# Kernel tuning notes

Measured on AMD Instinct MI355X. Metric: run time of the kernel, lower is better.

The kernel has to match this reference:

```python
import jax, jax.numpy as jnp
import numpy as np

B, N, C = 32, 4097, 256  # N odd so threshold length (N+1)//2 == N//2+1 rfft bins
F = N // 2 + 1


def setup_inputs() -> dict:
    key = jax.random.key(0)
    k1, k2, k3, k4 = jax.random.split(key, 4)
    x_in = jax.random.normal(k1, (B, N, C), dtype=jnp.float32)
    # trunc_normal(std=0.02) ~ scaled normal for reference purposes
    complex_weight = jax.random.normal(k2, (C, 2), dtype=jnp.float32) * 0.02
    complex_weight_high = jax.random.normal(k3, (C, 2), dtype=jnp.float32) * 0.02
    threshold_param = jax.random.uniform(k4, (F,), dtype=jnp.float32)
    return {
        "x_in": x_in,
        "complex_weight": complex_weight,
        "complex_weight_high": complex_weight_high,
        "threshold_param": threshold_param,
    }


def reference(x_in, complex_weight, complex_weight_high, threshold_param):
    dtype = x_in.dtype
    x = x_in.astype(jnp.float32)
    x_fft = jnp.fft.rfft(x, axis=1, norm="ortho")  # [B, F, C] complex64

    weight = complex_weight[:, 0] + 1j * complex_weight[:, 1]  # [C]
    x_weighted = x_fft * weight

    # adaptive high-frequency mask (straight-through on threshold_param)
    energy = jnp.sum(jnp.abs(x_fft) ** 2, axis=-1)  # [B, F]
    median_energy = jnp.median(energy, axis=1, keepdims=True)  # [B, 1] (F odd -> exact middle, matches torch)
    normalized_energy = energy / (median_energy + 1e-6)
    hard = (normalized_energy > threshold_param).astype(jnp.float32)  # [B, F]
    adaptive_mask = jax.lax.stop_gradient(hard - threshold_param) + threshold_param

    weight_high = complex_weight_high[:, 0] + 1j * complex_weight_high[:, 1]  # [C]
    x_weighted = x_weighted + x_fft * adaptive_mask[..., None] * weight_high

    out = jnp.fft.irfft(x_weighted, n=N, axis=1, norm="ortho")  # [B, N, C]
    return out.astype(dtype)
```

## Files before the change

### kernel.cpp

```cpp
#include <hip/hip_runtime.h>
#include <math.h>
#include <float.h>

#define B_ 32
#define N_ 4097
#define C_ 256
#define F_ 2049
#define N2_ 241
#define Q_ 512
#define TWROWS 4352
#define INV_SQRT_N 0.0156230927f
#define W_N 0.0015336063f
#define W_17 0.36959913571644626f

typedef __attribute__((ext_vector_type(8))) short short8v;
typedef _Float16 f16x8 __attribute__((ext_vector_type(8)));
typedef __attribute__((ext_vector_type(4))) float f32x4;

__device__ __forceinline__ float bf2f(unsigned short u) {
    return __uint_as_float(((unsigned)u) << 16);
}
__device__ __forceinline__ unsigned short f2bf(float v) {
    unsigned u = __float_as_uint(v);
    u += 0x7FFFu + ((u >> 16) & 1u);
    return (unsigned short)(u >> 16);
}
__device__ __forceinline__ unsigned short f2h(float v) {
    union { _Float16 h; unsigned short u; } cv;
    cv.h = (_Float16)v;
    return cv.u;
}
__device__ __forceinline__ void gload16(const void* gptr, void* ldsptr) {
    __builtin_amdgcn_global_load_lds(
        (const __attribute__((address_space(1))) void*)gptr,
        (__attribute__((address_space(3))) void*)ldsptr,
        16, 0, 0);
}

__global__ __launch_bounds__(256) void k_stageA_t(const float* __restrict__ x,
                                                  unsigned short* __restrict__ yt) {
    int bid = blockIdx.x;
    int b = bid >> 5; int rem = bid & 31;
    int n2t = rem >> 2, ct = rem & 3;
    int tid = threadIdx.x;
    int cl = tid & 63, sub = tid >> 6;
    int c = ct * 64 + cl;

    float C17[17], S17[17];
#pragma unroll
    for (int r = 0; r < 17; ++r) {
        float s, cth; sincosf(W_17 * (float)r, &s, &cth);
        C17[r] = cth; S17[r] = s;
    }

    float ar[9][8], ai[8][8];
#pragma unroll
    for (int k = 0; k < 9; ++k)
#pragma unroll
        for (int i = 0; i < 8; ++i) ar[k][i] = 0.f;
#pragma unroll
    for (int k = 0; k < 8; ++k)
#pragma unroll
        for (int i = 0; i < 8; ++i) ai[k][i] = 0.f;

    const float* xb = x + (size_t)b * N_ * C_ + c;
#pragma unroll
    for (int n1 = 0; n1 < 17; ++n1) {
        float xv[8];
#pragma unroll
        for (int i = 0; i < 8; ++i) {
            int n2 = n2t * 32 + sub * 8 + i;
            xv[i] = (n2 <= 240) ? xb[(size_t)(n1 * N2_ + n2) * C_] : 0.f;
        }
#pragma unroll
        for (int k1 = 0; k1 < 9; ++k1) {
            int r = (k1 * n1) % 17;
            float cc = C17[r], ss = S17[r];
#pragma unroll
            for (int i = 0; i < 8; ++i) {
                ar[k1][i] += xv[i] * cc;
                if (k1 > 0) ai[k1 - 1][i] += xv[i] * ss;
            }
        }
    }

    __shared__ float lre[32 * 65], lim[32 * 65];
    int c2 = tid >> 2, qg = tid & 3;
#pragma unroll
    for (int j = 0; j < 9; ++j) {
        __syncthreads();
#pragma unroll
        for (int i = 0; i < 8; ++i) {
            int row = sub * 8 + i;
            lre[row * 65 + cl] = ar[j][i] * INV_SQRT_N;
            lim[row * 65 + cl] = (j > 0) ? (-ai[j - 1][i] * INV_SQRT_N) : 0.f;
        }
        __syncthreads();
        unsigned wh[8];
#pragma unroll
        for (int i = 0; i < 8; ++i) {
            int row = qg * 8 + i;
            float re = lre[row * 65 + c2], im = lim[row * 65 + c2];
            wh[i] = (unsigned)f2h(re) | ((unsigned)f2h(im) << 16);
        }
        size_t ubase = ((size_t)((b * 9 + j) * 256 + ct * 64 + c2)) * 256 + n2t * 32 + qg * 8;
        uint4 v0; v0.x = wh[0]; v0.y = wh[1]; v0.z = wh[2]; v0.w = wh[3];
        uint4 v1; v1.x = wh[4]; v1.y = wh[5]; v1.z = wh[6]; v1.w = wh[7];
        *(uint4*)((unsigned*)yt + ubase) = v0;
        *(uint4*)((unsigned*)yt + ubase + 4) = v1;
    }
}

__global__ __launch_bounds__(256) void k_twfill_all(unsigned short* __restrict__ twA,
                                                    unsigned short* __restrict__ twB) {
    int blk = blockIdx.x;
    if (blk < TWROWS) {
        int n = blk;
        int k2 = threadIdx.x;
        unsigned pack = 0u;
        if (n <= 4096 && k2 <= 240) {
            int rr = (n * k2) % N_;
            float s, cth; sincosf(W_N * (float)rr, &s, &cth);
            pack = (unsigned)f2bf(cth) | ((unsigned)f2bf(-s) << 16);
        }
        *(unsigned*)(twA + (size_t)n * Q_ + 2 * k2) = pack;
    } else {
        int idx = blk - TWROWS;
        int m = idx & 255; int k1 = idx >> 8;
        int n2 = threadIdx.x;
        int t = m >> 1, r = m & 1;
        int f = k1 + 17 * t;
        unsigned ph = 0u;
        if (t <= 120 && f < F_ && n2 <= 240) {
            float s_ = (k1 <= 8) ? 1.f : -1.f;
            int rr = (f * n2) % N_;
            float sn, cs; sincosf(W_N * (float)rr, &sn, &cs);
            float a0 = (r == 0) ? cs : -sn;
            float a1 = (r == 0) ? s_ * sn : s_ * cs;
            ph = (unsigned)f2h(a0) | ((unsigned)f2h(a1) << 16);
        }
        size_t ub = ((size_t)(k1 * 256 + m)) * 256 + n2;
        *((unsigned*)twB + ub) = ph;
    }
}

__global__ __launch_bounds__(256) void k_stageB_v4(
        const unsigned short* __restrict__ yt, const unsigned short* __restrict__ twb,
        unsigned short* __restrict__ X, float* __restrict__ energy) {
    int bid = (blockIdx.x & 7) * 272 + (blockIdx.x >> 3);
    int b = bid / 68, rem = bid % 68;
    int j, mt, ct;
    if (rem < 4) { j = 0; mt = rem >> 1; ct = rem & 1; }
    else { int r2 = rem - 4; j = 1 + (r2 >> 3); int sub = r2 & 7; mt = sub >> 1; ct = sub & 1; }
    int k1 = (mt < 2) ? j : 17 - j;
    int mh = mt & 1;
    const unsigned short* pA = twb + (size_t)(k1 * 256 + mh * 128) * Q_;
    const unsigned short* pB = yt + (size_t)((b * 9 + j) * 256 + ct * 128) * Q_;

    int tid = threadIdx.x, lane = tid & 63, wid = tid >> 6;
    int wr = wid >> 1, wc = wid & 1;
    int l15 = lane & 15, lg = lane >> 4;
    int srow = lane >> 3, sch = lane & 7;

    __shared__ __align__(16) unsigned short lds[16384];
    __shared__ float eL[2][2][4][4][2];

    f32x4 acc[4][4];
#pragma unroll
    for (int rt = 0; rt < 4; ++rt)
#pragma unroll
        for (int nt = 0; nt < 4; ++nt) acc[rt][nt] = (f32x4){0.f, 0.f, 0.f, 0.f};

    for (int ks = 0; ks < 8; ++ks) {
        int q0 = ks * 64;
#pragma unroll
        for (int r = 0; r < 8; ++r) {
            int row = (r & 3) * 32 + wid * 8 + srow;
            int ch = sch ^ ((row >> 1) & 7);
            const unsigned short* g = (r < 4) ? (pA + (size_t)row * Q_ + q0 + ch * 8)
                                              : (pB + (size_t)row * Q_ + q0 + ch * 8);
            gload16(g, &lds[(r * 4 + wid) * 512]);
        }
        __syncthreads();
        f16x8 a[2][4], bb[2][4];
#pragma unroll
        for (int rt = 0; rt < 4; ++rt) {
            int row = wr * 64 + rt * 16 + l15;
            int s = (row >> 1) & 7;
            a[0][rt] = *(const f16x8*)&lds[(row * 8 + (lg ^ s)) * 8];
            a[1][rt] = *(const f16x8*)&lds[(row * 8 + ((4 + lg) ^ s)) * 8];
        }
#pragma unroll
        for (int nt = 0; nt < 4; ++nt) {
            int row = wc * 64 + nt * 16 + l15;
            int s = (row >> 1) & 7;
            bb[0][nt] = *(const f16x8*)&lds[8192 + (row * 8 + (lg ^ s)) * 8];
            bb[1][nt] = *(const f16x8*)&lds[8192 + (row * 8 + ((4 + lg) ^ s)) * 8];
        }
#pragma unroll
        for (int kh = 0; kh < 2; ++kh)
#pragma unroll
            for (int rt = 0; rt < 4; ++rt)
#pragma unroll
                for (int nt = 0; nt < 4; ++nt)
                    acc[rt][nt] = __builtin_amdgcn_mfma_f32_16x16x32_f16(
                        a[kh][rt], bb[kh][nt], acc[rt][nt], 0, 0, 0);
        __syncthreads();
    }

#pragma unroll
    for (int rt = 0; rt < 4; ++rt) {
        float e0 = 0.f, e1 = 0.f;
#pragma unroll
        for (int nt = 0; nt < 4; ++nt) {
            e0 += acc[rt][nt][0] * acc[rt][nt][0] + acc[rt][nt][1] * acc[rt][nt][1];
            e1 += acc[rt][nt][2] * acc[rt][nt][2] + acc[rt][nt][3] * acc[rt][nt][3];
        }
#pragma unroll
        for (int off = 1; off < 16; off <<= 1) {
            e0 += __shfl_xor(e0, off, 64);
            e1 += __shfl_xor(e1, off, 64);
        }
        if (l15 == 0) { eL[wr][wc][rt][lg][0] = e0; eL[wr][wc][rt][lg][1] = e1; }
    }
    __syncthreads();
    if (tid < 64) {
        int wr2 = tid >> 5, rt2 = (tid >> 3) & 3, lg2 = (tid >> 1) & 3, pr = tid & 1;
        int mrow = mh * 128 + wr2 * 64 + rt2 * 16 + lg2 * 4 + pr * 2;
        int f = k1 + 17 * (mrow >> 1);
        if (f < F_) {
            float e = eL[wr2][0][rt2][lg2][pr] + eL[wr2][1][rt2][lg2][pr];
            atomicAdd(&energy[b * F_ + f], e);
        }
    }

#pragma unroll
    for (int rt = 0; rt < 4; ++rt) {
#pragma unroll
        for (int jj = 0; jj < 4; ++jj) {
            int mrow = mh * 128 + wr * 64 + rt * 16 + lg * 4 + jj;
            int t = mrow >> 1, p = mrow & 1;
            int f = k1 + 17 * t;
            if (f < F_) {
                size_t base = ((size_t)((b * F_ + f) * 2 + p)) * C_ + ct * 128 + wc * 64 + l15;
#pragma unroll
                for (int nt = 0; nt < 4; ++nt)
                    X[base + nt * 16] = f2bf(acc[rt][nt][jj]);
            }
        }
    }
}

__global__ __launch_bounds__(256) void k_median(const float* __restrict__ energy,
                                                float* __restrict__ med) {
    int b = blockIdx.x, tid = threadIdx.x;
    __shared__ unsigned vals[F_];
    __shared__ unsigned hist[256];
    __shared__ unsigned scanbuf[256];
    __shared__ unsigned sh_prefix;
    __shared__ int sh_rank;
    for (int i = tid; i < F_; i += 256)
        vals[i] = __float_as_uint(energy[b * F_ + i]);
    if (tid == 0) { sh_prefix = 0u; sh_rank = 1024; }
    __syncthreads();
#pragma unroll
    for (int shift = 24; shift >= 0; shift -= 8) {
        hist[tid] = 0u;
        __syncthreads();
        unsigned prefix = sh_prefix;
        unsigned hmask = (shift == 24) ? 0u : (0xFFFFFFFFu << (shift + 8));
        for (int i = tid; i < F_; i += 256) {
            unsigned v = vals[i];
            if (((v ^ prefix) & hmask) == 0u)
                atomicAdd(&hist[(v >> shift) & 255], 1u);
        }
        __syncthreads();
        scanbuf[tid] = hist[tid];
        __syncthreads();
#pragma unroll
        for (int off = 1; off < 256; off <<= 1) {
            unsigned y = (tid >= off) ? scanbuf[tid - off] : 0u;
            __syncthreads();
            scanbuf[tid] += y;
            __syncthreads();
        }
        int rank = sh_rank;
        unsigned cumP = (tid == 0) ? 0u : scanbuf[tid - 1];
        unsigned cumI = scanbuf[tid];
        __syncthreads();
        if ((unsigned)rank >= cumP && (unsigned)rank < cumI) {
            sh_prefix = prefix | ((unsigned)tid << shift);
            sh_rank = rank - (int)cumP;
        }
        __syncthreads();
    }
    if (tid == 0) med[b] = __uint_as_float(sh_prefix);
}

__global__ __launch_bounds__(256) void k_vbuild_t(
        const unsigned short* __restrict__ X, const float* __restrict__ energy,
        const float* __restrict__ med, const float* __restrict__ thr,
        const float* __restrict__ cw, const float* __restrict__ cwh,
        unsigned short* __restrict__ vt) {
    int bid = blockIdx.x;
    int b = bid >> 7; int rem = bid & 127;
    int kt = rem >> 3, ct = rem & 7;
    int tid = threadIdx.x;
    int cl = tid & 31, ks = tid >> 5;
    int c = ct * 32 + cl;

    __shared__ unsigned stage[17 * 32 * 17];

    float wr = cw[2 * c], wi = cw[2 * c + 1];
    float whr = cwh[2 * c], whi = cwh[2 * c + 1];
    float denom = med[b] + 1e-6f;

    float C17[17], S17[17];
#pragma unroll
    for (int r = 0; r < 17; ++r) {
        float s, cth; sincosf(W_17 * (float)r, &s, &cth);
        C17[r] = cth; S17[r] = s;
    }

#pragma unroll
    for (int kk = 0; kk < 2; ++kk) {
        int klocal = kk * 8 + ks;
        int k2 = kt * 16 + klocal;
        float vr[17], vi[17];
#pragma unroll
        for (int m = 0; m < 17; ++m) { vr[m] = 0.f; vi[m] = 0.f; }
        if (k2 <= 240) {
#pragma unroll
            for (int s = 0; s < 9; ++s) {
                int f = k2 + 241 * s;
                if (f < F_) {
                    float e = energy[b * F_ + f];
                    float m = (e / denom > thr[f]) ? 1.0f : 0.0f;
                    float wer = wr + m * whr, wei = wi + m * whi;
                    float cf = ((f == 0) ? 1.0f : 2.0f) * INV_SQRT_N;
                    const unsigned short* Xrow = X + ((size_t)(b * F_ + f) * 2) * C_;
                    float Xr = bf2f(Xrow[c]), Xi = bf2f(Xrow[C_ + c]);
                    float Zr = (Xr * wer - Xi * wei) * cf;
                    float Zi = (Xr * wei + Xi * wer) * cf;
#pragma unroll
                    for (int m2 = 0; m2 < 17; ++m2) {
                        int r = (s * m2) % 17;
                        vr[m2] += Zr * C17[r] - Zi * S17[r];
                        vi[m2] += Zr * S17[r] + Zi * C17[r];
                    }
                }
            }
        }
#pragma unroll
        for (int m2 = 0; m2 < 17; ++m2)
            stage[(m2 * 32 + cl) * 17 + klocal] =
                (unsigned)f2bf(vr[m2]) | ((unsigned)f2bf(vi[m2]) << 16);
    }
    __syncthreads();
    unsigned* vt32 = (unsigned*)vt;
    for (int r = tid; r < 544; r += 256) {
        int m2 = r >> 5, c2 = r & 31;
        size_t ubase = ((size_t)((b * 17 + m2) * 256 + ct * 32 + c2)) * 256 + kt * 16;
        const unsigned* srow = &stage[(m2 * 32 + c2) * 17];
#pragma unroll
        for (int g = 0; g < 4; ++g) {
            uint4 w;
            w.x = srow[g * 4]; w.y = srow[g * 4 + 1];
            w.z = srow[g * 4 + 2]; w.w = srow[g * 4 + 3];
            *(uint4*)(vt32 + ubase + g * 4) = w;
        }
    }
}

__global__ __launch_bounds__(256) void k_stageC_v2(const short* __restrict__ vt,
                                                   const short* __restrict__ twA,
                                                   float* __restrict__ out) {
    int bid = (blockIdx.x & 7) * 272 + (blockIdx.x >> 3);
    int b = bid / 68, rem = bid % 68;
    int m2 = rem >> 2, mt = (rem >> 1) & 1, ct = rem & 1;

    int tid = threadIdx.x, lane = tid & 63, wid = tid >> 6;
    int wr = wid >> 1, wc = wid & 1;
    int l15 = lane & 15, lg = lane >> 4;
    int srow = lane >> 3, sch = lane & 7;

    const short* vtb = vt + (size_t)((b * 17 + m2) * 256 + ct * 128) * Q_;

    __shared__ __align__(16) short lds[16384];

    f32x4 acc[4][4];
#pragma unroll
    for (int rt = 0; rt < 4; ++rt)
#pragma unroll
        for (int nt = 0; nt < 4; ++nt) acc[rt][nt] = (f32x4){0.f, 0.f, 0.f, 0.f};

    for (int ks = 0; ks < 8; ++ks) {
        int q0 = ks * 64;
#pragma unroll
        for (int r = 0; r < 8; ++r) {
            int row = (r & 3) * 32 + wid * 8 + srow;
            int ch = sch ^ ((row >> 1) & 7);
            const short* g;
            if (r < 4) {
                int n = 17 * (mt * 128 + row) + m2;
                g = twA + (size_t)n * Q_ + q0 + ch * 8;
            } else {
                g = vtb + (size_t)row * Q_ + q0 + ch * 8;
            }
            gload16(g, &lds[(r * 4 + wid) * 512]);
        }
        __syncthreads();
        short8v a[2][4], bb[2][4];
#pragma unroll
        for (int rt = 0; rt < 4; ++rt) {
            int row = wr * 64 + rt * 16 + l15;
            int s = (row >> 1) & 7;
            a[0][rt] = *(const short8v*)&lds[(row * 8 + (lg ^ s)) * 8];
            a[1][rt] = *(const short8v*)&lds[(row * 8 + ((4 + lg) ^ s)) * 8];
        }
#pragma unroll
        for (int nt = 0; nt < 4; ++nt) {
            int row = wc * 64 + nt * 16 + l15;
            int s = (row >> 1) & 7;
            bb[0][nt] = *(const short8v*)&lds[8192 + (row * 8 + (lg ^ s)) * 8];
            bb[1][nt] = *(const short8v*)&lds[8192 + (row * 8 + ((4 + lg) ^ s)) * 8];
        }
#pragma unroll
        for (int kh = 0; kh < 2; ++kh)
#pragma unroll
            for (int rt = 0; rt < 4; ++rt)
#pragma unroll
                for (int nt = 0; nt < 4; ++nt)
                    acc[rt][nt] = __builtin_amdgcn_mfma_f32_16x16x32_bf16(
                        a[kh][rt], bb[kh][nt], acc[rt][nt], 0, 0, 0);
        __syncthreads();
    }

#pragma unroll
    for (int rt = 0; rt < 4; ++rt) {
#pragma unroll
        for (int jj = 0; jj < 4; ++jj) {
            int m1 = mt * 128 + wr * 64 + rt * 16 + lg * 4 + jj;
            if (m1 < N2_) {
                int n = 17 * m1 + m2;
                float* orow = out + ((size_t)b * N_ + n) * C_ + ct * 128 + wc * 64;
#pragma unroll
                for (int nt = 0; nt < 4; ++nt)
                    orow[nt * 16 + l15] = acc[rt][nt][jj];
            }
        }
    }
}

extern "C" void kernel_launch(void* const* d_in, const int* in_sizes, int n_in,
                              void* d_out, int out_size, void* d_ws, size_t ws_size,
                              hipStream_t stream) {
    const float* x   = (const float*)d_in[0];
    const float* cw  = (const float*)d_in[1];
    const float* cwh = (const float*)d_in[2];
    const float* thr = (const float*)d_in[3];
    float* out = (float*)d_out;

    char* ws = (char*)d_ws;
    unsigned short* Xb    = (unsigned short*)ws;
    char* sh = ws + 67141632ull;
    unsigned short* yt    = (unsigned short*)sh;
    unsigned short* vtb   = (unsigned short*)sh;
    char* tail = sh + 142606336ull;
    unsigned short* twA   = (unsigned short*)tail;
    unsigned short* twB   = (unsigned short*)(tail + 4456448ull);
    float* energy = (float*)(tail + 8912896ull);
    float* med    = (float*)(tail + 8912896ull + 262272ull);

    hipMemsetAsync(energy, 0, B_ * F_ * sizeof(float), stream);
    k_twfill_all<<<TWROWS + 17 * 256, 256, 0, stream>>>(twA, twB);
    k_stageA_t<<<B_ * 32, 256, 0, stream>>>(x, yt);
    k_stageB_v4<<<B_ * 68, 256, 0, stream>>>(yt, twB, Xb, energy);
    k_median<<<B_, 256, 0, stream>>>(energy, med);
    k_vbuild_t<<<B_ * 128, 256, 0, stream>>>(Xb, energy, med, thr, cw, cwh, vtb);
    k_stageC_v2<<<B_ * 68, 256, 0, stream>>>((const short*)vtb, (const short*)twA, out);
}
```

Baseline: 307.0 us.

## Double-buffer LDS tiles in both DFT GEMM stages to overlap loads with MFMA

Stage B and stage C GEMMs now use two 32-wide K tiles in LDS and prefetch the next tile while MFMAs run on the current one, instead of loading a 64-wide tile and syncing before compute. Global source pointers and LDS read offsets are precomputed outside the loop, and the swizzle is adapted to the narrower tile. The intent is to hide global-load latency behind the matrix ops. In exchange the loop has twice as many barriers and smaller K steps per sync.

```diff
diff --git a/kernel.cpp b/kernel.cpp
--- a/kernel.cpp
+++ b/kernel.cpp
@@ -144,7 +144,7 @@
     }
 }
 
-__global__ __launch_bounds__(256) void k_stageB_v4(
+__global__ __launch_bounds__(256) void k_stageB_v5(
         const unsigned short* __restrict__ yt, const unsigned short* __restrict__ twb,
         unsigned short* __restrict__ X, float* __restrict__ energy) {
     int bid = (blockIdx.x & 7) * 272 + (blockIdx.x >> 3);
@@ -160,53 +160,71 @@
     int tid = threadIdx.x, lane = tid & 63, wid = tid >> 6;
     int wr = wid >> 1, wc = wid & 1;
     int l15 = lane & 15, lg = lane >> 4;
-    int srow = lane >> 3, sch = lane & 7;
-
-    __shared__ __align__(16) unsigned short lds[16384];
+    int srow = lane >> 2, sch = lane & 3;
+
+    __shared__ __align__(16) unsigned short lds[2][8192];
     __shared__ float eL[2][2][4][4][2];
 
+    const unsigned short* gsrc[4];
+#pragma unroll
+    for (int r = 0; r < 4; ++r) {
+        int row = (r & 1) * 64 + wid * 16 + srow;
+        int ch = sch ^ ((row >> 1) & 3);
+        gsrc[r] = ((r < 2) ? pA : pB) + (size_t)row * Q_ + ch * 8;
+    }
+    int aoff[4], boff[4];
+#pragma unroll
+    for (int rt = 0; rt < 4; ++rt) {
+        int row = wr * 64 + rt * 16 + l15;
+        aoff[rt] = row * 32 + (lg ^ ((row >> 1) & 3)) * 8;
+    }
+#pragma unroll
+    for (int nt = 0; nt < 4; ++nt) {
+        int row = wc * 64 + nt * 16 + l15;
+        boff[nt] = 4096 + row * 32 + (lg ^ ((row >> 1) & 3)) * 8;
+    }
+
     f32x4 acc[4][4];
 #pragma unroll
     for (int rt = 0; rt < 4; ++rt)
 #pragma unroll
         for (int nt = 0; nt < 4; ++nt) acc[rt][nt] = (f32x4){0.f, 0.f, 0.f, 0.f};
 
-    for (int ks = 0; ks < 8; ++ks) {
-        int q0 = ks * 64;
-#pragma unroll
-        for (int r = 0; r < 8; ++r) {
-            int row = (r & 3) * 32 + wid * 8 + srow;
-            int ch = sch ^ ((row >> 1) & 7);
-            const unsigned short* g = (r < 4) ? (pA + (size_t)row * Q_ + q0 + ch * 8)
-                                              : (pB + (size_t)row * Q_ + q0 + ch * 8);
-            gload16(g, &lds[(r * 4 + wid) * 512]);
-        }
-        __syncthreads();
-        f16x8 a[2][4], bb[2][4];
-#pragma unroll
-        for (int rt = 0; rt < 4; ++rt) {
-            int row = wr * 64 + rt * 16 + l15;
-            int s = (row >> 1) & 7;
-            a[0][rt] = *(const f16x8*)&lds[(row * 8 + (lg ^ s)) * 8];
-            a[1][rt] = *(const f16x8*)&lds[(row * 8 + ((4 + lg) ^ s)) * 8];
-        }
-#pragma unroll
-        for (int nt = 0; nt < 4; ++nt) {
-            int row = wc * 64 + nt * 16 + l15;
-            int s = (row >> 1) & 7;
-            bb[0][nt] = *(const f16x8*)&lds[8192 + (row * 8 + (lg ^ s)) * 8];
-            bb[1][nt] = *(const f16x8*)&lds[8192 + (row * 8 + ((4 + lg) ^ s)) * 8];
-        }
-#pragma unroll
-        for (int kh = 0; kh < 2; ++kh)
-#pragma unroll
-            for (int rt = 0; rt < 4; ++rt)
-#pragma unroll
-                for (int nt = 0; nt < 4; ++nt)
-                    acc[rt][nt] = __builtin_amdgcn_mfma_f32_16x16x32_f16(
-                        a[kh][rt], bb[kh][nt], acc[rt][nt], 0, 0, 0);
-        __syncthreads();
-    }
+#define STAGE_B(bufi, q0) do {                                      \
+        gload16(gsrc[0] + (q0), &lds[bufi][wid * 512]);             \
+        gload16(gsrc[1] + (q0), &lds[bufi][2048 + wid * 512]);      \
+        gload16(gsrc[2] + (q0), &lds[bufi][4096 + wid * 512]);      \
+        gload16(gsrc[3] + (q0), &lds[bufi][6144 + wid * 512]);      \
+    } while (0)
+
+#define COMP_B(bufi) do {                                           \
+        f16x8 a_[4], b_[4];                                         \
+        _Pragma("unroll")                                           \
+        for (int rt = 0; rt < 4; ++rt)                              \
+            a_[rt] = *(const f16x8*)&lds[bufi][aoff[rt]];           \
+        _Pragma("unroll")                                           \
+        for (int nt = 0; nt < 4; ++nt)                              \
+            b_[nt] = *(const f16x8*)&lds[bufi][boff[nt]];           \
+        _Pragma("unroll")                                           \
+        for (int rt = 0; rt < 4; ++rt)                              \
+            _Pragma("unroll")                                       \
+            for (int nt = 0; nt < 4; ++nt)                          \
+                acc[rt][nt] = __builtin_amdgcn_mfma_f32_16x16x32_f16( \
+                    a_[rt], b_[nt], acc[rt][nt], 0, 0, 0);          \
+    } while (0)
+
+    STAGE_B(0, 0);
+    __syncthreads();
+    for (int ks = 0; ks < 16; ks += 2) {
+        STAGE_B(1, (ks + 1) * 32);
+        COMP_B(0);
+        __syncthreads();
+        if (ks + 2 < 16) STAGE_B(0, (ks + 2) * 32);
+        COMP_B(1);
+        __syncthreads();
+    }
+#undef STAGE_B
+#undef COMP_B
 
 #pragma unroll
     for (int rt = 0; rt < 4; ++rt) {
@@ -372,7 +390,7 @@
     }
 }
 
-__global__ __launch_bounds__(256) void k_stageC_v2(const short* __restrict__ vt,
+__global__ __launch_bounds__(256) void k_stageC_v3(const short* __restrict__ vt,
                                                    const short* __restrict__ twA,
                                                    float* __restrict__ out) {
     int bid = (blockIdx.x & 7) * 272 + (blockIdx.x >> 3);
@@ -382,11 +400,35 @@
     int tid = threadIdx.x, lane = tid & 63, wid = tid >> 6;
     int wr = wid >> 1, wc = wid & 1;
     int l15 = lane & 15, lg = lane >> 4;
-    int srow = lane >> 3, sch = lane & 7;
+    int srow = lane >> 2, sch = lane & 3;
 
     const short* vtb = vt + (size_t)((b * 17 + m2) * 256 + ct * 128) * Q_;
 
-    __shared__ __align__(16) short lds[16384];
+    __shared__ __align__(16) short lds[2][8192];
+
+    const short* gsrc[4];
+#pragma unroll
+    for (int r = 0; r < 4; ++r) {
+        int row = (r & 1) * 64 + wid * 16 + srow;
+        int ch = sch ^ ((row >> 1) & 3);
+        if (r < 2) {
+            int n = 17 * (mt * 128 + row) + m2;
+            gsrc[r] = twA + (size_t)n * Q_ + ch * 8;
+        } else {
+            gsrc[r] = vtb + (size_t)row * Q_ + ch * 8;
+        }
+    }
+    int aoff[4], boff[4];
+#pragma unroll
+    for (int rt = 0; rt < 4; ++rt) {
+        int row = wr * 64 + rt * 16 + l15;
+        aoff[rt] = row * 32 + (lg ^ ((row >> 1) & 3)) * 8;
+    }
+#pragma unroll
+    for (int nt = 0; nt < 4; ++nt) {
+        int row = wc * 64 + nt * 16 + l15;
+        boff[nt] = 4096 + row * 32 + (lg ^ ((row >> 1) & 3)) * 8;
+    }
 
     f32x4 acc[4][4];
 #pragma unroll
@@ -394,47 +436,41 @@
 #pragma unroll
         for (int nt = 0; nt < 4; ++nt) acc[rt][nt] = (f32x4){0.f, 0.f, 0.f, 0.f};
 
-    for (int ks = 0; ks < 8; ++ks) {
-        int q0 = ks * 64;
-#pragma unroll
-        for (int r = 0; r < 8; ++r) {
-            int row = (r & 3) * 32 + wid * 8 + srow;
-            int ch = sch ^ ((row >> 1) & 7);
-            const short* g;
-            if (r < 4) {
-                int n = 17 * (mt * 128 + row) + m2;
-                g = twA + (size_t)n * Q_ + q0 + ch * 8;
-            } else {
-                g = vtb + (size_t)row * Q_ + q0 + ch * 8;
-            }
-            gload16(g, &lds[(r * 4 + wid) * 512]);
-        }
-        __syncthreads();
-        short8v a[2][4], bb[2][4];
-#pragma unroll
-        for (int rt = 0; rt < 4; ++rt) {
-            int row = wr * 64 + rt * 16 + l15;
-            int s = (row >> 1) & 7;
-            a[0][rt] = *(const short8v*)&lds[(row * 8 + (lg ^ s)) * 8];
-            a[1][rt] = *(const short8v*)&lds[(row * 8 + ((4 + lg) ^ s)) * 8];
-        }
-#pragma unroll
-        for (int nt = 0; nt < 4; ++nt) {
-            int row = wc * 64 + nt * 16 + l15;
-            int s = (row >> 1) & 7;
-            bb[0][nt] = *(const short8v*)&lds[8192 + (row * 8 + (lg ^ s)) * 8];
-            bb[1][nt] = *(const short8v*)&lds[8192 + (row * 8 + ((4 + lg) ^ s)) * 8];
-        }
-#pragma unroll
-        for (int kh = 0; kh < 2; ++kh)
-#pragma unroll
-            for (int rt = 0; rt < 4; ++rt)
-#pragma unroll
-                for (int nt = 0; nt < 4; ++nt)
-                    acc[rt][nt] = __builtin_amdgcn_mfma_f32_16x16x32_bf16(
-                        a[kh][rt], bb[kh][nt], acc[rt][nt], 0, 0, 0);
-        __syncthreads();
-    }
+#define STAGE_C(bufi, q0) do {                                      \
+        gload16(gsrc[0] + (q0), &lds[bufi][wid * 512]);             \
+        gload16(gsrc[1] + (q0), &lds[bufi][2048 + wid * 512]);      \
+        gload16(gsrc[2] + (q0), &lds[bufi][4096 + wid * 512]);      \
+        gload16(gsrc[3] + (q0), &lds[bufi][6144 + wid * 512]);      \
+    } while (0)
+
+#define COMP_C(bufi) do {                                           \
+        short8v a_[4], b_[4];                                       \
+        _Pragma("unroll")                                           \
+        for (int rt = 0; rt < 4; ++rt)                              \
+            a_[rt] = *(const short8v*)&lds[bufi][aoff[rt]];         \
+        _Pragma("unroll")                                           \
+        for (int nt = 0; nt < 4; ++nt)                              \
+            b_[nt] = *(const short8v*)&lds[bufi][boff[nt]];         \
+        _Pragma("unroll")                                           \
+        for (int rt = 0; rt < 4; ++rt)                              \
+            _Pragma("unroll")                                       \
+            for (int nt = 0; nt < 4; ++nt)                          \
+                acc[rt][nt] = __builtin_amdgcn_mfma_f32_16x16x32_bf16( \
+                    a_[rt], b_[nt], acc[rt][nt], 0, 0, 0);          \
+    } while (0)
+
+    STAGE_C(0, 0);
+    __syncthreads();
+    for (int ks = 0; ks < 16; ks += 2) {
+        STAGE_C(1, (ks + 1) * 32);
+        COMP_C(0);
+        __syncthreads();
+        if (ks + 2 < 16) STAGE_C(0, (ks + 2) * 32);
+        COMP_C(1);
+        __syncthreads();
+    }
+#undef STAGE_C
+#undef COMP_C
 
 #pragma unroll
     for (int rt = 0; rt < 4; ++rt) {
@@ -475,8 +511,8 @@
     hipMemsetAsync(energy, 0, B_ * F_ * sizeof(float), stream);
     k_twfill_all<<<TWROWS + 17 * 256, 256, 0, stream>>>(twA, twB);
     k_stageA_t<<<B_ * 32, 256, 0, stream>>>(x, yt);
-    k_stageB_v4<<<B_ * 68, 256, 0, stream>>>(yt, twB, Xb, energy);
+    k_stageB_v5<<<B_ * 68, 256, 0, stream>>>(yt, twB, Xb, energy);
     k_median<<<B_, 256, 0, stream>>>(energy, med);
     k_vbuild_t<<<B_ * 128, 256, 0, stream>>>(Xb, energy, med, thr, cw, cwh, vtb);
-    k_stageC_v2<<<B_ * 68, 256, 0, stream>>>((const short*)vtb, (const short*)twA, out);
-}
+    k_stageC_v3<<<B_ * 68, 256, 0, stream>>>((const short*)vtb, (const short*)twA, out);
+}
```

Result: no change. 303.0 us (-1.3%).
